# Kernel tuning notes

Measured on AMD Instinct MI355X. Metric: run time of the kernel, lower is better.

Reference implementation:

```python
import jax, jax.numpy as jnp
import numpy as np
from jax import lax

B, L, R = 128, 256, 36
D_TXT, D_IMG, D_SOC = 768, 2048, 10
EPS = 0.05 ** 2        # geomloss blur=0.05, p=2 -> epsilon = blur^p
N_ITERS = 20           # fixed log-domain Sinkhorn iterations
GAMMA = 0.01


def _pcost(x, y):
    # x: [B,n,d], y: [B,m,d] -> C_ij = ||x_i - y_j||^2 / 2 (geomloss p=2 cost)
    xx = jnp.sum(x * x, -1)[:, :, None]
    yy = jnp.sum(y * y, -1)[:, None, :]
    xy = jnp.einsum('bnd,bmd->bnm', x, y)
    return 0.5 * (xx + yy - 2.0 * xy)


def _sinkhorn_cost(C, loga, logb, eps, n_iters):
    # Log-domain Sinkhorn; masked points carry loga/logb = -inf (zero weight).
    f = jnp.zeros(loga.shape, C.dtype)
    g = jnp.zeros(logb.shape, C.dtype)

    def body(fg, _):
        f, g = fg
        g = -eps * jax.nn.logsumexp(loga[:, :, None] + (f[:, :, None] - C) / eps, axis=1)
        f = -eps * jax.nn.logsumexp(logb[:, None, :] + (g[:, None, :] - C) / eps, axis=2)
        return (f, g), None

    (f, g), _ = lax.scan(body, (f, g), None, length=n_iters)
    a = jnp.exp(loga)  # exp(-inf) = 0 for masked entries
    b = jnp.exp(logb)
    return jnp.sum(a * f, -1) + jnp.sum(b * g, -1)  # <a,f> + <b,g>


def _forward(txt_global, txt_region, img_global, img_region, social, attn_mask,
             W_stat, b_stat, W_gt, b_gt, W_gi, b_gi, W_rt, b_rt, W_ri, b_ri,
             W_m1, b_m1, W_m2, b_m2):
    relu = jax.nn.relu
    soc = relu(social @ W_stat + b_stat)                            # [B,100]
    tg = relu(jnp.concatenate([txt_global, soc], axis=1) @ W_gt + b_gt)  # [B,200]
    ig = relu(img_global @ W_gi + b_gi)                              # [B,200]
    h = relu((tg + ig) @ W_m1 + b_m1)
    mix_pred = h @ W_m2 + b_m2                                       # [B,2]

    tr = relu(txt_region @ W_rt + b_rt)                              # [B,L,50]
    ir = relu(img_region @ W_ri + b_ri)                              # [B,R,50]

    Bn, _, _ = tr.shape
    Rn = ir.shape[1]
    mask = attn_mask > 0
    n_words = jnp.sum(attn_mask, axis=-1).astype(tr.dtype)          # [B]
    loga = jnp.where(mask, -jnp.log(n_words)[:, None], -jnp.inf)    # uniform over valid tokens
    logb = jnp.full((Bn, Rn), -jnp.log(float(Rn)), tr.dtype)        # uniform over regions

    # Debiased Sinkhorn divergence (geomloss SamplesLoss default debias=True):
    Sxy = _sinkhorn_cost(_pcost(tr, ir), loga, logb, EPS, N_ITERS)
    Sxx = _sinkhorn_cost(_pcost(tr, tr), loga, loga, EPS, N_ITERS)
    Syy = _sinkhorn_cost(_pcost(ir, ir), logb, logb, EPS, N_ITERS)
    w_dis = Sxy - 0.5 * (Sxx + Syy)                                  # [B]

    w_pred = jnp.stack([1.0 - GAMMA * w_dis, GAMMA * w_dis], axis=1)  # [B,2]
    logit = jax.nn.softmax(jnp.maximum(mix_pred, w_pred), axis=1)
    return logit


def setup_inputs() -> dict:
    key = jax.random.key(0)
    ks = jax.random.split(key, 24)
    init = lambda k, s: (jax.random.normal(k, s) * 0.02).astype(jnp.float32)
    lengths = jax.random.randint(ks[0], (B,), 16, L + 1)             # ragged lengths
    attn_mask = (jnp.arange(L)[None, :] < lengths[:, None]).astype(jnp.int32)
    return {
        'txt_global': jax.random.normal(ks[1], (B, D_TXT), jnp.float32),
        'txt_region': jax.random.normal(ks[2], (B, L, D_TXT), jnp.float32),
        'img_global': jax.random.normal(ks[3], (B, D_IMG), jnp.float32),
        'img_region': jax.random.normal(ks[4], (B, R, D_IMG), jnp.float32),
        'social': jax.random.normal(ks[5], (B, D_SOC), jnp.float32),
        'attn_mask': attn_mask,
        'W_stat': init(ks[6], (D_SOC, 100)), 'b_stat': jnp.zeros((100,), jnp.float32),
        'W_gt': init(ks[7], (868, 200)), 'b_gt': jnp.zeros((200,), jnp.float32),
        'W_gi': init(ks[8], (D_IMG, 200)), 'b_gi': jnp.zeros((200,), jnp.float32),
        'W_rt': init(ks[9], (D_TXT, 50)), 'b_rt': jnp.zeros((50,), jnp.float32),
        'W_ri': init(ks[10], (D_IMG, 50)), 'b_ri': jnp.zeros((50,), jnp.float32),
        'W_m1': init(ks[11], (200, 100)), 'b_m1': jnp.zeros((100,), jnp.float32),
        'W_m2': init(ks[12], (100, 2)), 'b_m2': jnp.zeros((2,), jnp.float32),
    }


def reference(txt_global, txt_region, img_global, img_region, social, attn_mask,
              W_stat, b_stat, W_gt, b_gt, W_gi, b_gi, W_rt, b_rt, W_ri, b_ri,
              W_m1, b_m1, W_m2, b_m2):
    return _forward(txt_global, txt_region, img_global, img_region, social, attn_mask,
                    W_stat, b_stat, W_gt, b_gt, W_gi, b_gi, W_rt, b_rt, W_ri, b_ri,
                    W_m1, b_m1, W_m2, b_m2)
```

## Files before the change

kernel.cpp:

```cpp
#include <hip/hip_runtime.h>

typedef float  f32x4 __attribute__((ext_vector_type(4)));
typedef short  s16x8 __attribute__((ext_vector_type(8)));

#define EPS_LN2      0.0017328679513998632f
#define INV_EPS_LN2  577.0780163555852f
#define LOG2_36      5.169925001442312f

__device__ __forceinline__ short f2bf(float x) {
  unsigned int u; __builtin_memcpy(&u, &x, 4);
  u = (u + 0x7FFFu + ((u >> 16) & 1u)) >> 16;
  return (short)u;
}

__global__ __launch_bounds__(256) void k_prep(
    const float* __restrict__ W_rt, const float* __restrict__ W_ri,
    short* __restrict__ frt, short* __restrict__ fri,
    const float* __restrict__ txt, const float* __restrict__ img,
    const float* __restrict__ social,
    const float* __restrict__ W_stat, const float* __restrict__ b_stat,
    const float* __restrict__ W_gt, const float* __restrict__ W_gi,
    float* __restrict__ pre) {
  __shared__ float sA[32][128];
  int bid = blockIdx.x;
  if (bid < 88) {
    int slot = bid * 256 + threadIdx.x;
    const float* W; short* dst; int f;
    if (slot < 6144) { W = W_rt; dst = frt; f = slot; }
    else             { W = W_ri; dst = fri; f = slot - 6144; }
    int k32 = f >> 8, rem = f & 255, ct = rem >> 6, l = rem & 63;
    int col = ct * 16 + (l & 15);
    int k0  = k32 * 32 + (l >> 4) * 8;
    s16x8 p;
#pragma unroll
    for (int c = 0; c < 8; ++c) {
      float v = (col < 50) ? W[(k0 + c) * 50 + col] : 0.f;
      p[c] = f2bf(v);
    }
    *(s16x8*)(dst + (long)f * 8) = p;
    return;
  }
  int gb = bid - 88;
  int job = gb >> 4, rb = (gb >> 2) & 3, cb = gb & 3;
  int t = threadIdx.x, r0 = rb * 32;
  const float* W; int k0, klen;
  if (job < 6)       { k0 = job * 128;       klen = 128; W = W_gt; }
  else if (job == 6) { k0 = 0;               klen = 100; W = W_gt + 768 * 200; }
  else               { k0 = (job - 7) * 128; klen = 128; W = W_gi; }
  if (job == 6) {
    for (int idx = t; idx < 4096; idx += 256) {
      int r = idx >> 7, k = idx & 127;
      float v = 0.f;
      if (k < 100) {
        v = b_stat[k];
#pragma unroll
        for (int u = 0; u < 10; ++u) v += social[(r0 + r) * 10 + u] * W_stat[u * 100 + k];
        v = fmaxf(v, 0.f);
      }
      sA[r][k] = v;
    }
  } else {
    const float* A = (job < 6) ? txt : img;
    int K_A = (job < 6) ? 768 : 2048;
    for (int idx = t; idx < 4096; idx += 256) {
      int r = idx >> 7, k = idx & 127;
      sA[r][k] = A[(r0 + r) * K_A + k0 + k];
    }
  }
  __syncthreads();
  int c = cb * 64 + (t & 63), rg = t >> 6;
  if (c < 200) {
    float acc[8];
#pragma unroll
    for (int i = 0; i < 8; ++i) acc[i] = 0.f;
    for (int k4 = 0; k4 < klen; k4 += 4) {
      float w0 = W[(k0 + k4    ) * 200 + c];
      float w1 = W[(k0 + k4 + 1) * 200 + c];
      float w2 = W[(k0 + k4 + 2) * 200 + c];
      float w3 = W[(k0 + k4 + 3) * 200 + c];
#pragma unroll
      for (int i = 0; i < 8; ++i) {
        f32x4 a = *(const f32x4*)&sA[rg * 8 + i][k4];
        acc[i] += a[0]*w0 + a[1]*w1 + a[2]*w2 + a[3]*w3;
      }
    }
    float* dst = pre + (long)job * 25600;
#pragma unroll
    for (int i = 0; i < 8; ++i)
      dst[(r0 + rg * 8 + i) * 200 + c] = acc[i];
  }
}

template<int K32>
__device__ __forceinline__ void proj_body(const float* __restrict__ A,
                                          const short* __restrict__ Bf,
                                          const float* __restrict__ bias,
                                          float* __restrict__ out, int bid) {
  int wave = threadIdx.x >> 6, lane = threadIdx.x & 63;
  int rl = lane & 15, q = lane >> 4;
  int row0 = bid * 64 + wave * 16;
  const int K = K32 * 32;
  const float* ar = A + (long)(row0 + rl) * K + q * 8;
  const s16x8* bp = (const s16x8*)Bf + lane;

  f32x4 acc[4];
#pragma unroll
  for (int ct = 0; ct < 4; ++ct) acc[ct] = (f32x4){0.f, 0.f, 0.f, 0.f};

  f32x4 a0 = *(const f32x4*)(ar);
  f32x4 a1 = *(const f32x4*)(ar + 4);
  s16x8 bf0 = bp[0], bf1 = bp[64], bf2 = bp[128], bf3 = bp[192];

  for (int k32 = 0; k32 < K32; ++k32) {
    f32x4 na0, na1;
    s16x8 nb0, nb1, nb2, nb3;
    if (k32 + 1 < K32) {
      na0 = *(const f32x4*)(ar + (k32 + 1) * 32);
      na1 = *(const f32x4*)(ar + (k32 + 1) * 32 + 4);
      const s16x8* nbp = bp + (k32 + 1) * 256;
      nb0 = nbp[0]; nb1 = nbp[64]; nb2 = nbp[128]; nb3 = nbp[192];
    }
    s16x8 af;
    af[0]=f2bf(a0[0]); af[1]=f2bf(a0[1]); af[2]=f2bf(a0[2]); af[3]=f2bf(a0[3]);
    af[4]=f2bf(a1[0]); af[5]=f2bf(a1[1]); af[6]=f2bf(a1[2]); af[7]=f2bf(a1[3]);
    acc[0] = __builtin_amdgcn_mfma_f32_16x16x32_bf16(af, bf0, acc[0], 0, 0, 0);
    acc[1] = __builtin_amdgcn_mfma_f32_16x16x32_bf16(af, bf1, acc[1], 0, 0, 0);
    acc[2] = __builtin_amdgcn_mfma_f32_16x16x32_bf16(af, bf2, acc[2], 0, 0, 0);
    acc[3] = __builtin_amdgcn_mfma_f32_16x16x32_bf16(af, bf3, acc[3], 0, 0, 0);
    a0 = na0; a1 = na1;
    bf0 = nb0; bf1 = nb1; bf2 = nb2; bf3 = nb3;
  }
#pragma unroll
  for (int ct = 0; ct < 4; ++ct) {
    int col = ct * 16 + rl;
    float bv = (col < 50) ? bias[col] : 0.f;
#pragma unroll
    for (int r = 0; r < 4; ++r) {
      int grow = row0 + q * 4 + r;
      float o = fmaxf(acc[ct][r] + bv, 0.f);
      out[(long)grow * 64 + col] = (col < 50) ? o : 0.f;
    }
  }
}

__device__ __forceinline__ void mix_body(
    int r, const float* __restrict__ pre,
    const float* __restrict__ b_gt, const float* __restrict__ b_gi,
    const float* __restrict__ W_m1, const float* __restrict__ b_m1,
    const float* __restrict__ W_m2, const float* __restrict__ b_m2,
    float* __restrict__ mix, float* smem) {
  float* sm = smem;
  float* sh = smem + 200;
  int t = threadIdx.x;
  if (t < 200) {
    float s1 = b_gt[t], s2 = b_gi[t];
#pragma unroll
    for (int j = 0; j < 7; ++j)  s1 += pre[(long)j * 25600 + r * 200 + t];
#pragma unroll
    for (int j = 7; j < 23; ++j) s2 += pre[(long)j * 25600 + r * 200 + t];
    sm[t] = fmaxf(s1, 0.f) + fmaxf(s2, 0.f);
  }
  __syncthreads();
  if (t < 100) {
    float a = b_m1[t];
#pragma unroll 4
    for (int k = 0; k < 200; ++k) a += sm[k] * W_m1[k * 100 + t];
    sh[t] = fmaxf(a, 0.f);
  }
  __syncthreads();
  if (t < 2) {
    float a = b_m2[t];
    for (int k = 0; k < 100; ++k) a += sh[k] * W_m2[k * 2 + t];
    mix[r * 2 + t] = a;
  }
}

__global__ __launch_bounds__(256)
__attribute__((amdgpu_waves_per_eu(4, 8)))
void k_pm(
    const float* __restrict__ txt_region, const short* __restrict__ frt,
    const float* __restrict__ b_rt, float* __restrict__ tr,
    const float* __restrict__ img_region, const short* __restrict__ fri,
    const float* __restrict__ b_ri, float* __restrict__ ir,
    const float* __restrict__ pre,
    const float* __restrict__ b_gt, const float* __restrict__ b_gi,
    const float* __restrict__ W_m1, const float* __restrict__ b_m1,
    const float* __restrict__ W_m2, const float* __restrict__ b_m2,
    float* __restrict__ mix) {
  __shared__ __align__(16) float smem[304];
  int bid = blockIdx.x;
  if (bid < 128)      mix_body(bid, pre, b_gt, b_gi, W_m1, b_m1, W_m2, b_m2, mix, smem);
  else if (bid < 640) proj_body<24>(txt_region, frt, b_rt, tr, bid - 128);
  else                proj_body<64>(img_region, fri, b_ri, ir, bid - 640);
}

#define SK_SMEM 50736

__global__ __launch_bounds__(1024)
__attribute__((amdgpu_waves_per_eu(4, 4)))
void k_sink(
    const float* __restrict__ tr, const float* __restrict__ ir,
    const int* __restrict__ amask, float* __restrict__ Cxx,
    float* __restrict__ Sxy, float* __restrict__ Sxx, float* __restrict__ Syy) {
  __shared__ __align__(16) char smem[SK_SMEM];
  int role = blockIdx.x >> 7;
  int b    = blockIdx.x & 127;
  int tid  = threadIdx.x;

  if (role == 0) {
    short* Xf    = (short*)smem;
    float* norms = (float*)(smem + 32768);
    float* sA    = (float*)(smem + 33792);
    float* sF    = (float*)(smem + 34816);
    float* sG    = (float*)(smem + 35840);
    float* sPm   = (float*)(smem + 36864);
    int*   nsh   = (int*)  (smem + 40960);
    if (tid < 64) {
      int c = 0;
      for (int i = tid; i < 256; i += 64) c += amask[b * 256 + i];
#pragma unroll
      for (int o = 1; o < 64; o <<= 1) c += __shfl_xor(c, o);
      if (tid == 0) *nsh = c;
    }
    const float* Xg = tr + (long)b * 256 * 64;
    for (int slot = tid; slot < 2048; slot += 1024) {
      int t = slot >> 7, k32 = (slot >> 6) & 1, l = slot & 63;
      int row = t * 16 + (l & 15), k0 = k32 * 32 + (l >> 4) * 8;
      const float* src = Xg + row * 64 + k0;
      f32x4 a0 = *(const f32x4*)src, a1 = *(const f32x4*)(src + 4);
      s16x8 p;
      p[0]=f2bf(a0[0]); p[1]=f2bf(a0[1]); p[2]=f2bf(a0[2]); p[3]=f2bf(a0[3]);
      p[4]=f2bf(a1[0]); p[5]=f2bf(a1[1]); p[6]=f2bf(a1[2]); p[7]=f2bf(a1[3]);
      *(s16x8*)(Xf + slot * 8) = p;
    }
    __syncthreads();
    int n = *nsh;
    int wv = tid >> 6, lane = tid & 63, q = lane >> 4;
    f32x4 acc[16];
#pragma unroll
    for (int ct = 0; ct < 16; ++ct) acc[ct] = (f32x4){0.f, 0.f, 0.f, 0.f};
    s16x8 afr0 = *(const s16x8*)(Xf + ((wv * 2 + 0) * 64 + lane) * 8);
    s16x8 afr1 = *(const s16x8*)(Xf + ((wv * 2 + 1) * 64 + lane) * 8);
#pragma unroll
    for (int ct = 0; ct < 16; ++ct) {
      s16x8 b0 = *(const s16x8*)(Xf + ((ct * 2 + 0) * 64 + lane) * 8);
      s16x8 b1 = *(const s16x8*)(Xf + ((ct * 2 + 1) * 64 + lane) * 8);
      acc[ct] = __builtin_amdgcn_mfma_f32_16x16x32_bf16(afr0, b0, acc[ct], 0, 0, 0);
      acc[ct] = __builtin_amdgcn_mfma_f32_16x16x32_bf16(afr1, b1, acc[ct], 0, 0, 0);
    }
#pragma unroll
    for (int r = 0; r < 4; ++r) {
      int m_ = q * 4 + r;
      if ((lane & 15) == m_) norms[wv * 16 + m_] = acc[wv][r];
    }
    __syncthreads();
    float* Cwb = Cxx + (long)b * 65536;
    if (wv * 16 < n) {
#pragma unroll
      for (int ct = 0; ct < 16; ++ct) {
        int gj = ct * 16 + (lane & 15);
        float nj = norms[gj];
#pragma unroll
        for (int r = 0; r < 4; ++r) {
          int gi = wv * 16 + q * 4 + r;
          Cwb[gi * 256 + gj] = (acc[ct][r] - 0.5f * (norms[gi] + nj)) * INV_EPS_LN2;
        }
      }
    }
    __syncthreads();
    int kk = tid >> 8, j = tid & 255, i0 = kk * 64;
    int iend = n - i0; if (iend > 64) iend = 64;
    float Creg[64];
    if (j < n) {
#pragma unroll
      for (int ch = 0; ch < 4; ++ch) {
        if (ch * 16 < iend) {
#pragma unroll
          for (int u = 0; u < 16; ++u)
            Creg[ch * 16 + u] = Cwb[(i0 + ch * 16 + u) * 256 + j];
        }
      }
    }
    float log2n = log2f((float)n);
    if (tid < 256) { sF[tid] = 0.f; sA[tid] = (tid < n) ? -log2n : -1e30f; }
    __syncthreads();
    const float* ap = sA + i0;
    for (int h = 0; h < 40; ++h) {
      float m = -1e30f;
      if (j < n) {
#pragma unroll
        for (int ch = 0; ch < 4; ++ch) {
          if (ch * 16 < iend) {
            const float* app = ap + ch * 16;
            f32x4 A0 = *(const f32x4*)(app);
            f32x4 A1 = *(const f32x4*)(app + 4);
            f32x4 A2 = *(const f32x4*)(app + 8);
            f32x4 A3 = *(const f32x4*)(app + 12);
            float x0 = A0[0]+Creg[ch*16+0],  x1 = A0[1]+Creg[ch*16+1];
            float x2 = A0[2]+Creg[ch*16+2],  x3 = A0[3]+Creg[ch*16+3];
            float x4 = A1[0]+Creg[ch*16+4],  x5 = A1[1]+Creg[ch*16+5];
            float x6 = A1[2]+Creg[ch*16+6],  x7 = A1[3]+Creg[ch*16+7];
            float x8 = A2[0]+Creg[ch*16+8],  x9 = A2[1]+Creg[ch*16+9];
            float xa = A2[2]+Creg[ch*16+10], xb = A2[3]+Creg[ch*16+11];
            float xc = A3[0]+Creg[ch*16+12], xd = A3[1]+Creg[ch*16+13];
            float xe = A3[2]+Creg[ch*16+14], xf = A3[3]+Creg[ch*16+15];
            float y0 = fmaxf(fmaxf(x0, x1), x2);
            float y1 = fmaxf(fmaxf(x3, x4), x5);
            float y2 = fmaxf(fmaxf(x6, x7), x8);
            float y3 = fmaxf(fmaxf(x9, xa), xb);
            float y4 = fmaxf(fmaxf(xc, xd), xe);
            float z0 = fmaxf(fmaxf(y0, y1), y2);
            float z1 = fmaxf(fmaxf(y3, y4), xf);
            m = fmaxf(fmaxf(m, z0), z1);
          }
        }
      }
      sPm[kk * 256 + j] = m;
      __syncthreads();
      if (tid < 256) {
        float m4 = fmaxf(fmaxf(sPm[tid], sPm[256 + tid]),
                         fmaxf(sPm[512 + tid], sPm[768 + tid]));
        if (tid < n) {
          ((h & 1) ? sF : sG)[tid] = -EPS_LN2 * m4;
          sA[tid] = -log2n - m4;
        }
      }
      __syncthreads();
    }
    if (tid < 64) {
      float a = 0.f;
      for (int i = tid; i < n; i += 64) a += sF[i] + sG[i];
#pragma unroll
      for (int o = 1; o < 64; o <<= 1) a += __shfl_xor(a, o);
      if (tid == 0) Sxx[b] = a / n;
    }
  } else if (role == 1) {
    float* Ys  = (float*)smem;
    float* Cs  = (float*)(smem + 9216);
    float* nx  = (float*)(smem + 47104);
    float* ny  = (float*)(smem + 48128);
    float* sA  = (float*)(smem + 48288);
    float* sB  = (float*)(smem + 49376);
    float* sF  = (float*)(smem + 49536);
    float* sG  = (float*)(smem + 50560);
    int*   nsh = (int*)  (smem + 50720);
    if (tid < 64) {
      int c = 0;
      for (int i = tid; i < 256; i += 64) c += amask[b * 256 + i];
#pragma unroll
      for (int o = 1; o < 64; o <<= 1) c += __shfl_xor(c, o);
      if (tid == 0) *nsh = c;
    }
    const float* Xg = tr + (long)b * 256 * 64;
    const float* Yg = ir + (long)b * 36 * 64;
    for (int idx = tid; idx < 576; idx += 1024) {
      int row = idx >> 4, q4 = idx & 15;
      *(f32x4*)(Ys + row * 64 + q4 * 4) = *(const f32x4*)(Yg + row * 64 + q4 * 4);
    }
    __syncthreads();
    int n = *nsh;
    if (tid < 256) {
      float a = 0.f;
#pragma unroll
      for (int q4 = 0; q4 < 13; ++q4) {
        f32x4 v = *(const f32x4*)(Xg + tid * 64 + q4 * 4);
        a += v[0]*v[0] + v[1]*v[1] + v[2]*v[2] + v[3]*v[3];
      }
      nx[tid] = a;
    } else if (tid < 292) {
      int jj = tid - 256; float a = 0.f;
#pragma unroll
      for (int q4 = 0; q4 < 13; ++q4) {
        f32x4 v = *(const f32x4*)(Ys + jj * 64 + q4 * 4);
        a += v[0]*v[0] + v[1]*v[1] + v[2]*v[2] + v[3]*v[3];
      }
      ny[jj] = a;
    }
    __syncthreads();
    if (tid < 1008) {
      int ii = tid / 36, jj = tid - ii * 36;
      f32x4 yr[13];
#pragma unroll
      for (int q4 = 0; q4 < 13; ++q4) yr[q4] = *(const f32x4*)(Ys + jj * 64 + q4 * 4);
      float nyj = ny[jj];
      for (int i = ii; i < 256; i += 28) {
        float d = 0.f;
#pragma unroll
        for (int q4 = 0; q4 < 13; ++q4) {
          f32x4 xv = *(const f32x4*)(Xg + i * 64 + q4 * 4);
          d += xv[0]*yr[q4][0] + xv[1]*yr[q4][1] + xv[2]*yr[q4][2] + xv[3]*yr[q4][3];
        }
        Cs[i * 37 + jj] = (d - 0.5f * (nx[i] + nyj)) * INV_EPS_LN2;
      }
    }
    __syncthreads();
    int jg = tid >> 4, kg = tid & 15;
    float Cg[16];
    if (jg < 36) {
#pragma unroll
      for (int t = 0; t < 16; ++t) Cg[t] = Cs[(kg * 16 + t) * 37 + jg];
    }
    int fi = tid >> 2, kf = tid & 3;
    float Cf[9];
#pragma unroll
    for (int t = 0; t < 9; ++t) {
      int jj2 = kf * 9 + t;
      Cf[t] = (jj2 < 36) ? Cs[fi * 37 + jj2] : 0.f;
    }
    float log2n = log2f((float)n);
    if (tid < 256) { sF[tid] = 0.f; sA[tid + (tid >> 4)] = -log2n; }
    __syncthreads();
    const float* agp = sA + kg * 17;
    int gend = n - kg * 16; if (gend > 16) gend = 16;
    for (int it = 0; it < 20; ++it) {
      float gm = -1e30f;
      if (jg < 36) {
#pragma unroll
        for (int t = 0; t < 16; ++t)
          if (t < gend) gm = fmaxf(gm, agp[t] + Cg[t]);
        gm = fmaxf(gm, __shfl_xor(gm, 1)); gm = fmaxf(gm, __shfl_xor(gm, 2));
        gm = fmaxf(gm, __shfl_xor(gm, 4)); gm = fmaxf(gm, __shfl_xor(gm, 8));
      }
      __syncthreads();
      if (jg < 36 && kg == 0) {
        sG[jg] = -EPS_LN2 * gm;
        sB[jg] = -LOG2_36 - gm;
      }
      __syncthreads();
      float fm = -1e30f;
#pragma unroll
      for (int t = 0; t < 9; ++t) {
        int jj2 = kf * 9 + t;
        if (jj2 < 36) fm = fmaxf(fm, sB[jj2] + Cf[t]);
      }
      fm = fmaxf(fm, __shfl_xor(fm, 1)); fm = fmaxf(fm, __shfl_xor(fm, 2));
      __syncthreads();
      if (kf == 0 && fi < n) {
        sF[fi] = -EPS_LN2 * fm;
        sA[fi + (fi >> 4)] = -log2n - fm;
      }
      __syncthreads();
    }
    if (tid < 64) {
      float a = 0.f;
      for (int i = tid; i < n; i += 64) a += sF[i];
      float g = (tid < 36) ? sG[tid] : 0.f;
#pragma unroll
      for (int o = 1; o < 64; o <<= 1) { a += __shfl_xor(a, o); g += __shfl_xor(g, o); }
      if (tid == 0) Sxy[b] = a / n + g / 36.f;
    }
  } else {
    float* Ys = (float*)smem;
    float* Cs = (float*)(smem + 9216);
    float* ny = (float*)(smem + 48128);
    float* sA = (float*)(smem + 48288);
    float* sF = (float*)(smem + 49536);
    float* sG = (float*)(smem + 50560);
    const float* Yg = ir + (long)b * 36 * 64;
    for (int idx = tid; idx < 576; idx += 1024) {
      int row = idx >> 4, q4 = idx & 15;
      *(f32x4*)(Ys + row * 64 + q4 * 4) = *(const f32x4*)(Yg + row * 64 + q4 * 4);
    }
    __syncthreads();
    if (tid < 36) {
      float a = 0.f;
#pragma unroll
      for (int q4 = 0; q4 < 13; ++q4) {
        f32x4 v = *(const f32x4*)(Ys + tid * 64 + q4 * 4);
        a += v[0]*v[0] + v[1]*v[1] + v[2]*v[2] + v[3]*v[3];
      }
      ny[tid] = a;
    }
    __syncthreads();
    if (tid < 1008) {
      int ii = tid / 36, jj = tid - ii * 36;
      f32x4 yr[13];
#pragma unroll
      for (int q4 = 0; q4 < 13; ++q4) yr[q4] = *(const f32x4*)(Ys + jj * 64 + q4 * 4);
      float nyj = ny[jj];
      for (int i = ii; i < 36; i += 28) {
        float d = 0.f;
#pragma unroll
        for (int q4 = 0; q4 < 13; ++q4) {
          f32x4 xv = *(const f32x4*)(Ys + i * 64 + q4 * 4);
          d += xv[0]*yr[q4][0] + xv[1]*yr[q4][1] + xv[2]*yr[q4][2] + xv[3]*yr[q4][3];
        }
        Cs[i * 37 + jj] = (d - 0.5f * (ny[i] + nyj)) * INV_EPS_LN2;
      }
    }
    __syncthreads();
    int j = tid >> 2, kk = tid & 3;
    float Creg[9];
    if (j < 36) {
#pragma unroll
      for (int t = 0; t < 9; ++t) {
        int i2 = kk * 9 + t;
        Creg[t] = (i2 < 36) ? Cs[i2 * 37 + j] : 0.f;
      }
    }
    if (tid < 36) { sF[tid] = 0.f; sA[tid] = -LOG2_36; }
    __syncthreads();
    for (int h = 0; h < 40; ++h) {
      float m = -1e30f;
      if (j < 36) {
#pragma unroll
        for (int t = 0; t < 9; ++t) {
          int i2 = kk * 9 + t;
          if (i2 < 36) m = fmaxf(m, sA[i2] + Creg[t]);
        }
        m = fmaxf(m, __shfl_xor(m, 1)); m = fmaxf(m, __shfl_xor(m, 2));
      }
      __syncthreads();
      if (j < 36 && kk == 0) {
        ((h & 1) ? sF : sG)[j] = -EPS_LN2 * m;
        sA[j] = -LOG2_36 - m;
      }
      __syncthreads();
    }
    if (tid < 64) {
      float a = (tid < 36) ? sF[tid] + sG[tid] : 0.f;
#pragma unroll
      for (int o = 1; o < 64; o <<= 1) a += __shfl_xor(a, o);
      if (tid == 0) Syy[b] = a / 36.f;
    }
  }
}

__global__ void k_final(const float* __restrict__ mix, const float* __restrict__ sxy,
                        const float* __restrict__ sxx, const float* __restrict__ syy,
                        float* __restrict__ out) {
  int b = blockIdx.x * 64 + threadIdx.x;
  if (b < 128) {
    float w  = sxy[b] - 0.5f * (sxx[b] + syy[b]);
    float x0 = fmaxf(mix[b * 2 + 0], 1.0f - 0.01f * w);
    float x1 = fmaxf(mix[b * 2 + 1], 0.01f * w);
    float mx = fmaxf(x0, x1);
    float e0 = expf(x0 - mx), e1 = expf(x1 - mx);
    float inv = 1.f / (e0 + e1);
    out[b * 2 + 0] = e0 * inv;
    out[b * 2 + 1] = e1 * inv;
  }
}

extern "C" void kernel_launch(void* const* d_in, const int* in_sizes, int n_in,
                              void* d_out, int out_size, void* d_ws, size_t ws_size,
                              hipStream_t stream) {
  const float* txt_global = (const float*)d_in[0];
  const float* txt_region = (const float*)d_in[1];
  const float* img_global = (const float*)d_in[2];
  const float* img_region = (const float*)d_in[3];
  const float* social     = (const float*)d_in[4];
  const int*   attn_mask  = (const int*)  d_in[5];
  const float* W_stat = (const float*)d_in[6];  const float* b_stat = (const float*)d_in[7];
  const float* W_gt   = (const float*)d_in[8];  const float* b_gt   = (const float*)d_in[9];
  const float* W_gi   = (const float*)d_in[10]; const float* b_gi   = (const float*)d_in[11];
  const float* W_rt   = (const float*)d_in[12]; const float* b_rt   = (const float*)d_in[13];
  const float* W_ri   = (const float*)d_in[14]; const float* b_ri   = (const float*)d_in[15];
  const float* W_m1   = (const float*)d_in[16]; const float* b_m1   = (const float*)d_in[17];
  const float* W_m2   = (const float*)d_in[18]; const float* b_m2   = (const float*)d_in[19];

  float* ws = (float*)d_ws;
  float* ws_mix = ws;
  float* ws_sxy = ws + 256;
  float* ws_sxx = ws + 384;
  float* ws_syy = ws + 512;
  short* ws_frt = (short*)(ws + 1024);
  short* ws_fri = (short*)(ws + 25600);
  float* ws_tr  = ws + 131072;
  float* ws_ir  = ws + 2228224;
  float* ws_cxx = ws + 2523136;
  float* ws_pre = ws_cxx;

  k_prep<<<456, 256, 0, stream>>>(W_rt, W_ri, ws_frt, ws_fri,
                                  txt_global, img_global, social,
                                  W_stat, b_stat, W_gt, W_gi, ws_pre);
  k_pm<<<712, 256, 0, stream>>>(txt_region, ws_frt, b_rt, ws_tr,
                                img_region, ws_fri, b_ri, ws_ir,
                                ws_pre, b_gt, b_gi,
                                W_m1, b_m1, W_m2, b_m2, ws_mix);
  k_sink<<<384, 1024, 0, stream>>>(ws_tr, ws_ir, attn_mask, ws_cxx,
                                   ws_sxy, ws_sxx, ws_syy);
  k_final<<<2, 64, 0, stream>>>(ws_mix, ws_sxy, ws_sxx, ws_syy, (float*)d_out);
}
```

Measured before the change: 336.3 us.

## Split-K projection GEMM across wave pairs with deeper register prefetch

The region projection kernel now splits the K dimension across two waves per 16-row group and reduces the partial accumulators through shared memory. This halves the rows per block and roughly doubles the block count, which exposes more parallelism for the memory-bound fp32 input streaming. The K loop is fully unrolled with a 3-deep register prefetch ring instead of single-step double buffering. Block order is changed so the long image blocks launch first, and the waves-per-EU cap is tightened. The cost is an extra barrier, shared-memory reduction traffic and higher register pressure.

```diff
diff --git a/kernel.cpp b/kernel.cpp
--- a/kernel.cpp
+++ b/kernel.cpp
@@ -95,50 +95,70 @@
 __device__ __forceinline__ void proj_body(const float* __restrict__ A,
                                           const short* __restrict__ Bf,
                                           const float* __restrict__ bias,
-                                          float* __restrict__ out, int bid) {
+                                          float* __restrict__ out, int bid,
+                                          float* __restrict__ red) {
+  constexpr int KH = K32 / 2;
+  constexpr int D  = 3;
   int wave = threadIdx.x >> 6, lane = threadIdx.x & 63;
+  int rg = wave >> 1, ks = wave & 1;
   int rl = lane & 15, q = lane >> 4;
-  int row0 = bid * 64 + wave * 16;
+  int row0 = bid * 32 + rg * 16;
   const int K = K32 * 32;
-  const float* ar = A + (long)(row0 + rl) * K + q * 8;
-  const s16x8* bp = (const s16x8*)Bf + lane;
-
+  const float* ar = A + (long)(row0 + rl) * K + ks * (KH * 32) + q * 8;
+  const s16x8* bp = (const s16x8*)Bf + ks * (KH * 256) + lane;
+
+  f32x4 pa0[D], pa1[D];
+  s16x8 pb0[D], pb1[D], pb2[D], pb3[D];
+#pragma unroll
+  for (int d = 0; d < D; ++d) {
+    pa0[d] = *(const f32x4*)(ar + d * 32);
+    pa1[d] = *(const f32x4*)(ar + d * 32 + 4);
+    const s16x8* p = bp + d * 256;
+    pb0[d] = p[0]; pb1[d] = p[64]; pb2[d] = p[128]; pb3[d] = p[192];
+  }
   f32x4 acc[4];
 #pragma unroll
   for (int ct = 0; ct < 4; ++ct) acc[ct] = (f32x4){0.f, 0.f, 0.f, 0.f};
 
-  f32x4 a0 = *(const f32x4*)(ar);
-  f32x4 a1 = *(const f32x4*)(ar + 4);
-  s16x8 bf0 = bp[0], bf1 = bp[64], bf2 = bp[128], bf3 = bp[192];
-
-  for (int k32 = 0; k32 < K32; ++k32) {
-    f32x4 na0, na1;
-    s16x8 nb0, nb1, nb2, nb3;
-    if (k32 + 1 < K32) {
-      na0 = *(const f32x4*)(ar + (k32 + 1) * 32);
-      na1 = *(const f32x4*)(ar + (k32 + 1) * 32 + 4);
-      const s16x8* nbp = bp + (k32 + 1) * 256;
-      nb0 = nbp[0]; nb1 = nbp[64]; nb2 = nbp[128]; nb3 = nbp[192];
-    }
+#pragma unroll
+  for (int k32 = 0; k32 < KH; ++k32) {
+    int slot = k32 % D;
     s16x8 af;
-    af[0]=f2bf(a0[0]); af[1]=f2bf(a0[1]); af[2]=f2bf(a0[2]); af[3]=f2bf(a0[3]);
-    af[4]=f2bf(a1[0]); af[5]=f2bf(a1[1]); af[6]=f2bf(a1[2]); af[7]=f2bf(a1[3]);
-    acc[0] = __builtin_amdgcn_mfma_f32_16x16x32_bf16(af, bf0, acc[0], 0, 0, 0);
-    acc[1] = __builtin_amdgcn_mfma_f32_16x16x32_bf16(af, bf1, acc[1], 0, 0, 0);
-    acc[2] = __builtin_amdgcn_mfma_f32_16x16x32_bf16(af, bf2, acc[2], 0, 0, 0);
-    acc[3] = __builtin_amdgcn_mfma_f32_16x16x32_bf16(af, bf3, acc[3], 0, 0, 0);
-    a0 = na0; a1 = na1;
-    bf0 = nb0; bf1 = nb1; bf2 = nb2; bf3 = nb3;
-  }
-#pragma unroll
-  for (int ct = 0; ct < 4; ++ct) {
-    int col = ct * 16 + rl;
-    float bv = (col < 50) ? bias[col] : 0.f;
-#pragma unroll
-    for (int r = 0; r < 4; ++r) {
-      int grow = row0 + q * 4 + r;
-      float o = fmaxf(acc[ct][r] + bv, 0.f);
-      out[(long)grow * 64 + col] = (col < 50) ? o : 0.f;
+    af[0]=f2bf(pa0[slot][0]); af[1]=f2bf(pa0[slot][1]);
+    af[2]=f2bf(pa0[slot][2]); af[3]=f2bf(pa0[slot][3]);
+    af[4]=f2bf(pa1[slot][0]); af[5]=f2bf(pa1[slot][1]);
+    af[6]=f2bf(pa1[slot][2]); af[7]=f2bf(pa1[slot][3]);
+    acc[0] = __builtin_amdgcn_mfma_f32_16x16x32_bf16(af, pb0[slot], acc[0], 0, 0, 0);
+    acc[1] = __builtin_amdgcn_mfma_f32_16x16x32_bf16(af, pb1[slot], acc[1], 0, 0, 0);
+    acc[2] = __builtin_amdgcn_mfma_f32_16x16x32_bf16(af, pb2[slot], acc[2], 0, 0, 0);
+    acc[3] = __builtin_amdgcn_mfma_f32_16x16x32_bf16(af, pb3[slot], acc[3], 0, 0, 0);
+    if (k32 + D < KH) {
+      pa0[slot] = *(const f32x4*)(ar + (k32 + D) * 32);
+      pa1[slot] = *(const f32x4*)(ar + (k32 + D) * 32 + 4);
+      const s16x8* p = bp + (k32 + D) * 256;
+      pb0[slot] = p[0]; pb1[slot] = p[64]; pb2[slot] = p[128]; pb3[slot] = p[192];
+    }
+  }
+
+  float* rb = red + rg * 1024;
+  if (ks == 1) {
+#pragma unroll
+    for (int ct = 0; ct < 4; ++ct)
+      *(f32x4*)(rb + lane * 16 + ct * 4) = acc[ct];
+  }
+  __syncthreads();
+  if (ks == 0) {
+#pragma unroll
+    for (int ct = 0; ct < 4; ++ct) {
+      f32x4 o = *(const f32x4*)(rb + lane * 16 + ct * 4);
+      int col = ct * 16 + rl;
+      float bv = (col < 50) ? bias[col] : 0.f;
+#pragma unroll
+      for (int r = 0; r < 4; ++r) {
+        int grow = row0 + q * 4 + r;
+        float v = fmaxf(acc[ct][r] + o[r] + bv, 0.f);
+        out[(long)grow * 64 + col] = (col < 50) ? v : 0.f;
+      }
     }
   }
 }
@@ -176,7 +196,7 @@
 }
 
 __global__ __launch_bounds__(256)
-__attribute__((amdgpu_waves_per_eu(4, 8)))
+__attribute__((amdgpu_waves_per_eu(4, 4)))
 void k_pm(
     const float* __restrict__ txt_region, const short* __restrict__ frt,
     const float* __restrict__ b_rt, float* __restrict__ tr,
@@ -187,11 +207,11 @@
     const float* __restrict__ W_m1, const float* __restrict__ b_m1,
     const float* __restrict__ W_m2, const float* __restrict__ b_m2,
     float* __restrict__ mix) {
-  __shared__ __align__(16) float smem[304];
+  __shared__ __align__(16) float smem[2048];
   int bid = blockIdx.x;
-  if (bid < 128)      mix_body(bid, pre, b_gt, b_gi, W_m1, b_m1, W_m2, b_m2, mix, smem);
-  else if (bid < 640) proj_body<24>(txt_region, frt, b_rt, tr, bid - 128);
-  else                proj_body<64>(img_region, fri, b_ri, ir, bid - 640);
+  if (bid < 144)       proj_body<64>(img_region, fri, b_ri, ir, bid, smem);
+  else if (bid < 1168) proj_body<24>(txt_region, frt, b_rt, tr, bid - 144, smem);
+  else                 mix_body(bid - 1168, pre, b_gt, b_gi, W_m1, b_m1, W_m2, b_m2, mix, smem);
 }
 
 #define SK_SMEM 50736
@@ -574,10 +594,10 @@
   k_prep<<<456, 256, 0, stream>>>(W_rt, W_ri, ws_frt, ws_fri,
                                   txt_global, img_global, social,
                                   W_stat, b_stat, W_gt, W_gi, ws_pre);
-  k_pm<<<712, 256, 0, stream>>>(txt_region, ws_frt, b_rt, ws_tr,
-                                img_region, ws_fri, b_ri, ws_ir,
-                                ws_pre, b_gt, b_gi,
-                                W_m1, b_m1, W_m2, b_m2, ws_mix);
+  k_pm<<<1296, 256, 0, stream>>>(txt_region, ws_frt, b_rt, ws_tr,
+                                 img_region, ws_fri, b_ri, ws_ir,
+                                 ws_pre, b_gt, b_gi,
+                                 W_m1, b_m1, W_m2, b_m2, ws_mix);
   k_sink<<<384, 1024, 0, stream>>>(ws_tr, ws_ir, attn_mask, ws_cxx,
                                    ws_sxy, ws_sxx, ws_syy);
   k_final<<<2, 64, 0, stream>>>(ws_mix, ws_sxy, ws_sxx, ws_syy, (float*)d_out);
```

Result: faster. 322.2 us (-4.2%).

## Stage projection operands through LDS with async loads and pin Sinkhorn cost tiles in registers

Applied to the files above, without the earlier changes.

The region-projection GEMM now uses global_load_lds to double-buffer A and B tiles in shared memory, with a block barrier each k-step. Before, each wave prefetched its operands straight into registers. The block order in k_pm changes so the long image projections start first, and the waves_per_eu hint is dropped. In the Sinkhorn self-term, the per-thread cost column is loaded unconditionally into 16 vector registers, with an asm barrier to keep them resident and avoid spills or rematerialization from the Creg array. The added per-iteration barriers and extra LDS use may lower occupancy.

```diff
diff --git a/kernel.cpp b/kernel.cpp
--- a/kernel.cpp
+++ b/kernel.cpp
@@ -12,6 +12,10 @@
   u = (u + 0x7FFFu + ((u >> 16) & 1u)) >> 16;
   return (short)u;
 }
+
+#define GLOAD16(g, l) __builtin_amdgcn_global_load_lds( \
+    (const __attribute__((address_space(1))) void*)(g), \
+    (__attribute__((address_space(3))) void*)(l), 16, 0, 0)
 
 __global__ __launch_bounds__(256) void k_prep(
     const float* __restrict__ W_rt, const float* __restrict__ W_ri,
@@ -95,50 +99,59 @@
 __device__ __forceinline__ void proj_body(const float* __restrict__ A,
                                           const short* __restrict__ Bf,
                                           const float* __restrict__ bias,
-                                          float* __restrict__ out, int bid) {
+                                          float* __restrict__ out, int bid,
+                                          char* smem) {
+  char* abuf = smem;
+  char* bbuf = smem + 16384;
   int wave = threadIdx.x >> 6, lane = threadIdx.x & 63;
   int rl = lane & 15, q = lane >> 4;
-  int row0 = bid * 64 + wave * 16;
+  int row0 = bid * 64;
   const int K = K32 * 32;
-  const float* ar = A + (long)(row0 + rl) * K + q * 8;
-  const s16x8* bp = (const s16x8*)Bf + lane;
+  const float* arow = A + (long)(row0 + wave * 16 + rl) * K + q * 8;
+  const short* brow = Bf + wave * 512 + lane * 8;
+
+#define PROJ_STAGE(KK, PH) { \
+    const float* asrc = arow + (KK) * 32; \
+    char* ad = abuf + (PH) * 8192 + wave * 2048; \
+    GLOAD16(asrc,     ad); \
+    GLOAD16(asrc + 4, ad + 1024); \
+    GLOAD16(brow + (long)(KK) * 2048, bbuf + (PH) * 4096 + wave * 1024); \
+  }
 
   f32x4 acc[4];
 #pragma unroll
   for (int ct = 0; ct < 4; ++ct) acc[ct] = (f32x4){0.f, 0.f, 0.f, 0.f};
 
-  f32x4 a0 = *(const f32x4*)(ar);
-  f32x4 a1 = *(const f32x4*)(ar + 4);
-  s16x8 bf0 = bp[0], bf1 = bp[64], bf2 = bp[128], bf3 = bp[192];
-
-  for (int k32 = 0; k32 < K32; ++k32) {
-    f32x4 na0, na1;
-    s16x8 nb0, nb1, nb2, nb3;
-    if (k32 + 1 < K32) {
-      na0 = *(const f32x4*)(ar + (k32 + 1) * 32);
-      na1 = *(const f32x4*)(ar + (k32 + 1) * 32 + 4);
-      const s16x8* nbp = bp + (k32 + 1) * 256;
-      nb0 = nbp[0]; nb1 = nbp[64]; nb2 = nbp[128]; nb3 = nbp[192];
-    }
+  PROJ_STAGE(0, 0);
+  __syncthreads();
+
+  for (int k = 0; k < K32; ++k) {
+    if (k + 1 < K32) PROJ_STAGE(k + 1, (k + 1) & 1);
+    const char* ab = abuf + (k & 1) * 8192 + wave * 2048 + lane * 16;
+    const char* bb = bbuf + (k & 1) * 4096 + lane * 16;
+    f32x4 a0 = *(const f32x4*)(ab);
+    f32x4 a1 = *(const f32x4*)(ab + 1024);
     s16x8 af;
     af[0]=f2bf(a0[0]); af[1]=f2bf(a0[1]); af[2]=f2bf(a0[2]); af[3]=f2bf(a0[3]);
     af[4]=f2bf(a1[0]); af[5]=f2bf(a1[1]); af[6]=f2bf(a1[2]); af[7]=f2bf(a1[3]);
-    acc[0] = __builtin_amdgcn_mfma_f32_16x16x32_bf16(af, bf0, acc[0], 0, 0, 0);
-    acc[1] = __builtin_amdgcn_mfma_f32_16x16x32_bf16(af, bf1, acc[1], 0, 0, 0);
-    acc[2] = __builtin_amdgcn_mfma_f32_16x16x32_bf16(af, bf2, acc[2], 0, 0, 0);
-    acc[3] = __builtin_amdgcn_mfma_f32_16x16x32_bf16(af, bf3, acc[3], 0, 0, 0);
-    a0 = na0; a1 = na1;
-    bf0 = nb0; bf1 = nb1; bf2 = nb2; bf3 = nb3;
-  }
+#pragma unroll
+    for (int ct = 0; ct < 4; ++ct) {
+      s16x8 bfr = *(const s16x8*)(bb + ct * 1024);
+      acc[ct] = __builtin_amdgcn_mfma_f32_16x16x32_bf16(af, bfr, acc[ct], 0, 0, 0);
+    }
+    __syncthreads();
+  }
+#undef PROJ_STAGE
+
 #pragma unroll
   for (int ct = 0; ct < 4; ++ct) {
     int col = ct * 16 + rl;
     float bv = (col < 50) ? bias[col] : 0.f;
 #pragma unroll
     for (int r = 0; r < 4; ++r) {
-      int grow = row0 + q * 4 + r;
-      float o = fmaxf(acc[ct][r] + bv, 0.f);
-      out[(long)grow * 64 + col] = (col < 50) ? o : 0.f;
+      int grow = row0 + wave * 16 + q * 4 + r;
+      float v = fmaxf(acc[ct][r] + bv, 0.f);
+      out[(long)grow * 64 + col] = (col < 50) ? v : 0.f;
     }
   }
 }
@@ -176,7 +189,6 @@
 }
 
 __global__ __launch_bounds__(256)
-__attribute__((amdgpu_waves_per_eu(4, 8)))
 void k_pm(
     const float* __restrict__ txt_region, const short* __restrict__ frt,
     const float* __restrict__ b_rt, float* __restrict__ tr,
@@ -187,11 +199,11 @@
     const float* __restrict__ W_m1, const float* __restrict__ b_m1,
     const float* __restrict__ W_m2, const float* __restrict__ b_m2,
     float* __restrict__ mix) {
-  __shared__ __align__(16) float smem[304];
+  __shared__ __align__(16) char smem[24576];
   int bid = blockIdx.x;
-  if (bid < 128)      mix_body(bid, pre, b_gt, b_gi, W_m1, b_m1, W_m2, b_m2, mix, smem);
-  else if (bid < 640) proj_body<24>(txt_region, frt, b_rt, tr, bid - 128);
-  else                proj_body<64>(img_region, fri, b_ri, ir, bid - 640);
+  if (bid < 72)       proj_body<64>(img_region, fri, b_ri, ir, bid, smem);
+  else if (bid < 584) proj_body<24>(txt_region, frt, b_rt, tr, bid - 72, smem);
+  else                mix_body(bid - 584, pre, b_gt, b_gi, W_m1, b_m1, W_m2, b_m2, mix, (float*)smem);
 }
 
 #define SK_SMEM 50736
@@ -270,50 +282,48 @@
     __syncthreads();
     int kk = tid >> 8, j = tid & 255, i0 = kk * 64;
     int iend = n - i0; if (iend > 64) iend = 64;
-    float Creg[64];
-    if (j < n) {
-#pragma unroll
-      for (int ch = 0; ch < 4; ++ch) {
-        if (ch * 16 < iend) {
-#pragma unroll
-          for (int u = 0; u < 16; ++u)
-            Creg[ch * 16 + u] = Cwb[(i0 + ch * 16 + u) * 256 + j];
-        }
-      }
+    f32x4 c0, c1, c2, c3, c4, c5, c6, c7, c8, c9, ca, cb, cc, cd, ce, cf;
+    if (i0 < n) {
+      const float* cp = Cwb + (long)i0 * 256 + j;
+#define XXLD(CV, T0) \
+      CV[0] = cp[(T0+0)*256]; CV[1] = cp[(T0+1)*256]; \
+      CV[2] = cp[(T0+2)*256]; CV[3] = cp[(T0+3)*256];
+      XXLD(c0, 0)  XXLD(c1, 4)  XXLD(c2, 8)  XXLD(c3, 12)
+      XXLD(c4, 16) XXLD(c5, 20) XXLD(c6, 24) XXLD(c7, 28)
+      XXLD(c8, 32) XXLD(c9, 36) XXLD(ca, 40) XXLD(cb, 44)
+      XXLD(cc, 48) XXLD(cd, 52) XXLD(ce, 56) XXLD(cf, 60)
+#undef XXLD
+      asm volatile("" : "+v"(c0), "+v"(c1), "+v"(c2), "+v"(c3),
+                        "+v"(c4), "+v"(c5), "+v"(c6), "+v"(c7),
+                        "+v"(c8), "+v"(c9), "+v"(ca), "+v"(cb),
+                        "+v"(cc), "+v"(cd), "+v"(ce), "+v"(cf));
     }
     float log2n = log2f((float)n);
     if (tid < 256) { sF[tid] = 0.f; sA[tid] = (tid < n) ? -log2n : -1e30f; }
     __syncthreads();
-    const float* ap = sA + i0;
+    const float* ap2 = sA + i0;
+#define XXG(CA, CB, CC, CD, OFF) { \
+      f32x4 A0 = *(const f32x4*)(ap2 + OFF); \
+      f32x4 A1 = *(const f32x4*)(ap2 + OFF + 4); \
+      f32x4 A2 = *(const f32x4*)(ap2 + OFF + 8); \
+      f32x4 A3 = *(const f32x4*)(ap2 + OFF + 12); \
+      float x0 = A0[0]+CA[0], x1 = A0[1]+CA[1], x2 = A0[2]+CA[2], x3 = A0[3]+CA[3]; \
+      float x4 = A1[0]+CB[0], x5 = A1[1]+CB[1], x6 = A1[2]+CB[2], x7 = A1[3]+CB[3]; \
+      float x8 = A2[0]+CC[0], x9 = A2[1]+CC[1], xa = A2[2]+CC[2], xb = A2[3]+CC[3]; \
+      float xc = A3[0]+CD[0], xd = A3[1]+CD[1], xe = A3[2]+CD[2], xf = A3[3]+CD[3]; \
+      float y0 = fmaxf(fmaxf(x0, x1), x2); \
+      float y1 = fmaxf(fmaxf(x3, x4), x5); \
+      float y2 = fmaxf(fmaxf(x6, x7), x8); \
+      float y3 = fmaxf(fmaxf(x9, xa), xb); \
+      float y4 = fmaxf(fmaxf(xc, xd), xe); \
+      m = fmaxf(m, fmaxf(fmaxf(fmaxf(y0, y1), fmaxf(y2, y3)), fmaxf(y4, xf))); }
     for (int h = 0; h < 40; ++h) {
       float m = -1e30f;
-      if (j < n) {
-#pragma unroll
-        for (int ch = 0; ch < 4; ++ch) {
-          if (ch * 16 < iend) {
-            const float* app = ap + ch * 16;
-            f32x4 A0 = *(const f32x4*)(app);
-            f32x4 A1 = *(const f32x4*)(app + 4);
-            f32x4 A2 = *(const f32x4*)(app + 8);
-            f32x4 A3 = *(const f32x4*)(app + 12);
-            float x0 = A0[0]+Creg[ch*16+0],  x1 = A0[1]+Creg[ch*16+1];
-            float x2 = A0[2]+Creg[ch*16+2],  x3 = A0[3]+Creg[ch*16+3];
-            float x4 = A1[0]+Creg[ch*16+4],  x5 = A1[1]+Creg[ch*16+5];
-            float x6 = A1[2]+Creg[ch*16+6],  x7 = A1[3]+Creg[ch*16+7];
-            float x8 = A2[0]+Creg[ch*16+8],  x9 = A2[1]+Creg[ch*16+9];
-            float xa = A2[2]+Creg[ch*16+10], xb = A2[3]+Creg[ch*16+11];
-            float xc = A3[0]+Creg[ch*16+12], xd = A3[1]+Creg[ch*16+13];
-            float xe = A3[2]+Creg[ch*16+14], xf = A3[3]+Creg[ch*16+15];
-            float y0 = fmaxf(fmaxf(x0, x1), x2);
-            float y1 = fmaxf(fmaxf(x3, x4), x5);
-            float y2 = fmaxf(fmaxf(x6, x7), x8);
-            float y3 = fmaxf(fmaxf(x9, xa), xb);
-            float y4 = fmaxf(fmaxf(xc, xd), xe);
-            float z0 = fmaxf(fmaxf(y0, y1), y2);
-            float z1 = fmaxf(fmaxf(y3, y4), xf);
-            m = fmaxf(fmaxf(m, z0), z1);
-          }
-        }
+      if (i0 < n && j < n) {
+        XXG(c0, c1, c2, c3, 0)
+        if (iend > 16) { XXG(c4, c5, c6, c7, 16) }
+        if (iend > 32) { XXG(c8, c9, ca, cb, 32) }
+        if (iend > 48) { XXG(cc, cd, ce, cf, 48) }
       }
       sPm[kk * 256 + j] = m;
       __syncthreads();
@@ -327,6 +337,7 @@
       }
       __syncthreads();
     }
+#undef XXG
     if (tid < 64) {
       float a = 0.f;
       for (int i = tid; i < n; i += 64) a += sF[i] + sG[i];
```

Result: no change. 336.0 us (-0.1%).
